# Optimization experiments

Hardware: AMD Instinct MI355X
Metric: run time of the kernel (lower is better)

The kernel has to match this reference:

```python
import jax, jax.numpy as jnp
import numpy as np

B, T, N, F_IN = 8, 288, 2000, 1
E, ID, H, K = 128, 16, 128, 20
FL = T // 2 + 1  # rfft length = in_len//2 + 1
EPS_NORM = 1e-12
EPS_LN = 1e-8


def setup_inputs() -> dict:
    key = jax.random.key(0)
    k0, k1, k2, k3, k4 = jax.random.split(key, 5)
    return {
        "x": jax.random.normal(k0, (B, T, N, F_IN), jnp.float32),
        "Ex": jax.random.normal(k1, (FL, E), jnp.float32),
        "nodes": jax.random.normal(k2, (N, ID), jnp.float32),
        "Wd": jax.random.normal(k3, (N, E + ID, H), jnp.float32),
        "Wxabs": jax.random.normal(k4, (H, H), jnp.float32),
    }


def reference(x, Ex, nodes, Wd, Wxabs):
    # [B,T,N,F] -> take feature 0 -> [B,N,T]
    xt = jnp.transpose(x[:, :, :, 0], (0, 2, 1))
    xf = jnp.abs(jnp.fft.rfft(xt, axis=-1))  # [B,N,FL]
    # F.normalize p=2 over dim=1 (nodes), then dim=2 (freq): x / max(||x||, eps)
    xf = xf / jnp.clip(jnp.sqrt(jnp.sum(xf * xf, axis=1, keepdims=True)), EPS_NORM)
    xf = xf / jnp.clip(jnp.sqrt(jnp.sum(xf * xf, axis=2, keepdims=True)), EPS_NORM)
    xe = jnp.matmul(xf, Ex)  # [B,N,E]
    # cat(): append static node identity embedding per batch element
    xk = jnp.concatenate(
        [xe, jnp.broadcast_to(nodes, (xe.shape[0], N, ID))], axis=-1
    )  # [B,N,E+ID]
    # per-node weight bmm: [N,B,E+ID] @ [N,E+ID,H] -> [B,N,H]
    x1 = jax.nn.relu(jnp.einsum('bnd,ndh->bnh', xk, Wd))
    # LayerNorm over last two dims [N,H], eps=1e-8, no affine
    mu = jnp.mean(x1, axis=(1, 2), keepdims=True)
    var = jnp.mean((x1 - mu) ** 2, axis=(1, 2), keepdims=True)
    x2 = (x1 - mu) / jnp.sqrt(var + EPS_LN)
    # dropout is identity at inference
    adp = jnp.einsum('bnh,hk->bnk', x2, Wxabs)  # convt
    adj = jnp.einsum('bnh,bmh->bnm', adp, x1)  # [B,N,N]
    adp = jax.nn.relu(adj)
    # dy_mask_graph: per-row topk over dim=2 (torch dim=1 of the [N,N] slice),
    # binary mask via scatter of ones, then elementwise mask
    _, idx = jax.lax.top_k(adp, K)  # [B,N,K]
    bi = jnp.arange(adp.shape[0])[:, None, None]
    ni = jnp.arange(N)[None, :, None]
    mask = jnp.zeros_like(adp).at[bi, ni, idx].set(1.0)
    adj_masked = adp * mask
    return jax.nn.softmax(adj_masked, axis=2)
```

## Files before the change

### kernel.cpp

```cpp
#include <hip/hip_runtime.h>
#include <math.h>

#define BB 8
#define TT 288
#define NN 2000
#define FLEN 145
#define EE 128
#define IDD 16
#define HH 128
#define DKK 144
#define KTOP 20

typedef _Float16 half8 __attribute__((ext_vector_type(8)));
typedef float f32x4 __attribute__((ext_vector_type(4)));
typedef unsigned short ushort_t;

#define OFF_TW  ((size_t)0)
#define SZ_TW   ((size_t)TT*FLEN*2)
#define OFF_XF  (OFF_TW + SZ_TW)
#define SZ_XF   ((size_t)BB*FLEN*NN)
#define OFF_ICN (OFF_XF + SZ_XF)
#define OFF_IRN (OFF_ICN + (size_t)BB*FLEN)
#define OFF_XE  (OFF_IRN + (size_t)BB*NN)
#define SZ_BNH  ((size_t)BB*NN*HH)
#define OFF_X1  (OFF_XE + SZ_BNH)
#define OFF_ADP (OFF_X1 + SZ_BNH)
#define OFF_CSW (OFF_ADP + SZ_BNH)
#define OFF_LNS (OFF_CSW + HH)
#define OFF_LNF (OFF_LNS + 16)

__device__ __forceinline__ float wredSum(float v) {
#pragma unroll
  for (int o = 32; o > 0; o >>= 1) v += __shfl_down(v, o, 64);
  return v;
}
__device__ __forceinline__ float wredMax(float v) {
#pragma unroll
  for (int o = 32; o > 0; o >>= 1) v = fmaxf(v, __shfl_down(v, o, 64));
  return v;
}

__device__ __forceinline__ void split16(float v, ushort_t& hi, ushort_t& lo) {
  _Float16 h = (_Float16)v;
  _Float16 l = (_Float16)(v - (float)h);
  union { _Float16 f; ushort_t u; } a, b;
  a.f = h; b.f = l;
  hi = a.u; lo = b.u;
}

__global__ void k_init(const float* __restrict__ Wx, float* __restrict__ csw,
                       float* __restrict__ lns) {
  int k = threadIdx.x;
  float s = 0.f;
  for (int h = 0; h < HH; ++h) s += Wx[h * HH + k];
  csw[k] = s;
  if (k < 16) lns[k] = 0.f;
}

__global__ void k_tw(float* __restrict__ tw) {
  int id = blockIdx.x * 256 + threadIdx.x;
  if (id >= TT * FLEN) return;
  int t = id / FLEN, f = id % FLEN;
  int r = (t * f) % TT;
  double th = -2.0 * 3.14159265358979323846 * (double)r / (double)TT;
  tw[2 * id]     = (float)cos(th);
  tw[2 * id + 1] = (float)sin(th);
}

__global__ void k_dft(const float* __restrict__ x, const float* __restrict__ tw,
                      float* __restrict__ xf) {
  __shared__ __align__(16) float Xs[16][128];
  __shared__ __align__(16) float TWs[16][32][2];
  const int b = blockIdx.z;
  const int f0 = blockIdx.y * 32;
  const int n0 = blockIdx.x * 128;
  const int tid = threadIdx.x;
  const int tn = tid & 31;
  const int tf = tid >> 5;
  float ar[4][4] = {}, ai[4][4] = {};
  for (int t0 = 0; t0 < TT; t0 += 16) {
    __syncthreads();
    for (int l = tid; l < 512; l += 256) {
      int row = l >> 5, q = l & 31;
      int n = n0 + q * 4;
      const float* src = x + ((size_t)b * TT + (t0 + row)) * NN + n;
      float4 v = make_float4(0, 0, 0, 0);
      if (n + 3 < NN) v = *(const float4*)src;
      else {
        if (n + 0 < NN) v.x = src[0];
        if (n + 1 < NN) v.y = src[1];
        if (n + 2 < NN) v.z = src[2];
        if (n + 3 < NN) v.w = src[3];
      }
      *(float4*)&Xs[row][q * 4] = v;
    }
    for (int l = tid; l < 512; l += 256) {
      int row = l >> 5, ff = l & 31;
      int f = f0 + ff;
      float2 cs = make_float2(0, 0);
      if (f < FLEN) cs = *(const float2*)&tw[((size_t)(t0 + row) * FLEN + f) * 2];
      *(float2*)&TWs[row][ff][0] = cs;
    }
    __syncthreads();
#pragma unroll 4
    for (int t = 0; t < 16; ++t) {
      float4 xv = *(float4*)&Xs[t][tn * 4];
      float xx[4] = {xv.x, xv.y, xv.z, xv.w};
      float4 p0 = *(float4*)&TWs[t][tf * 4][0];
      float4 p1 = *(float4*)&TWs[t][tf * 4 + 2][0];
      float c[4] = {p0.x, p0.z, p1.x, p1.z};
      float s[4] = {p0.y, p0.w, p1.y, p1.w};
#pragma unroll
      for (int i = 0; i < 4; ++i)
#pragma unroll
        for (int j = 0; j < 4; ++j) {
          ar[i][j] = fmaf(xx[j], c[i], ar[i][j]);
          ai[i][j] = fmaf(xx[j], s[i], ai[i][j]);
        }
    }
  }
#pragma unroll
  for (int i = 0; i < 4; ++i) {
    int f = f0 + tf * 4 + i;
    if (f >= FLEN) continue;
    float* dst = &xf[((size_t)b * FLEN + f) * NN];
    float o[4];
#pragma unroll
    for (int j = 0; j < 4; ++j)
      o[j] = sqrtf(ar[i][j] * ar[i][j] + ai[i][j] * ai[i][j]);
    int n = n0 + tn * 4;
    if (n + 3 < NN) *(float4*)&dst[n] = make_float4(o[0], o[1], o[2], o[3]);
    else {
#pragma unroll
      for (int j = 0; j < 4; ++j) if (n + j < NN) dst[n + j] = o[j];
    }
  }
}

__global__ void k_colnorm(const float* __restrict__ xf, float* __restrict__ icn) {
  __shared__ float sc[4];
  int bf = blockIdx.x;
  const float* rowp = xf + (size_t)bf * NN;
  float s = 0.f;
  for (int i = threadIdx.x; i < NN; i += 256) { float v = rowp[i]; s = fmaf(v, v, s); }
  s = wredSum(s);
  int lane = threadIdx.x & 63, w = threadIdx.x >> 6;
  if (lane == 0) sc[w] = s;
  __syncthreads();
  if (threadIdx.x == 0)
    icn[bf] = 1.f / fmaxf(sqrtf(sc[0] + sc[1] + sc[2] + sc[3]), 1e-12f);
}

__global__ void k_rownorm(const float* __restrict__ xf, const float* __restrict__ icn,
                          float* __restrict__ irn) {
  int b = blockIdx.y;
  int n = blockIdx.x * 256 + threadIdx.x;
  if (n >= NN) return;
  float s = 0.f;
  for (int f = 0; f < FLEN; ++f) {
    float v = xf[((size_t)b * FLEN + f) * NN + n] * icn[b * FLEN + f];
    s = fmaf(v, v, s);
  }
  irn[b * NN + n] = 1.f / fmaxf(sqrtf(s), 1e-12f);
}

__global__ void k_xe(const float* __restrict__ xf, const float* __restrict__ icn,
                     const float* __restrict__ irn, const float* __restrict__ Ex,
                     float* __restrict__ xe) {
  __shared__ __align__(16) float As[16][64];
  __shared__ __align__(16) float Bs[16][128];
  const int b = blockIdx.y;
  const int n0 = blockIdx.x * 64;
  const int tid = threadIdx.x;
  const int tn = tid >> 4, te = tid & 15;
  float acc[4][8] = {};
  for (int f0 = 0; f0 < 160; f0 += 16) {
    __syncthreads();
    {
      int kt = tid >> 4, q = tid & 15;
      int f = f0 + kt;
      int n = n0 + q * 4;
      float4 v = make_float4(0, 0, 0, 0);
      if (f < FLEN) {
        float ic = icn[b * FLEN + f];
        const float* src = &xf[((size_t)b * FLEN + f) * NN + n];
        if (n + 3 < NN) v = *(const float4*)src;
        else {
          if (n + 0 < NN) v.x = src[0];
          if (n + 1 < NN) v.y = src[1];
          if (n + 2 < NN) v.z = src[2];
          if (n + 3 < NN) v.w = src[3];
        }
        v.x *= ic; v.y *= ic; v.z *= ic; v.w *= ic;
      }
      *(float4*)&As[kt][q * 4] = v;
    }
    for (int l = tid; l < 512; l += 256) {
      int kt = l >> 5, q = l & 31;
      int f = f0 + kt;
      float4 v = make_float4(0, 0, 0, 0);
      if (f < FLEN) v = *(const float4*)&Ex[(size_t)f * EE + q * 4];
      *(float4*)&Bs[kt][q * 4] = v;
    }
    __syncthreads();
#pragma unroll
    for (int k = 0; k < 16; ++k) {
      float4 a  = *(float4*)&As[k][tn * 4];
      float4 b0 = *(float4*)&Bs[k][te * 4];
      float4 b1 = *(float4*)&Bs[k][64 + te * 4];
      float av[4] = {a.x, a.y, a.z, a.w};
      float bv[8] = {b0.x, b0.y, b0.z, b0.w, b1.x, b1.y, b1.z, b1.w};
#pragma unroll
      for (int i = 0; i < 4; ++i)
#pragma unroll
        for (int j = 0; j < 8; ++j)
          acc[i][j] = fmaf(av[i], bv[j], acc[i][j]);
    }
  }
#pragma unroll
  for (int i = 0; i < 4; ++i) {
    int n = n0 + tn * 4 + i;
    if (n >= NN) continue;
    float sc = irn[b * NN + n];
    float* dst = &xe[((size_t)b * NN + n) * EE];
    *(float4*)&dst[te * 4] =
        make_float4(acc[i][0] * sc, acc[i][1] * sc, acc[i][2] * sc, acc[i][3] * sc);
    *(float4*)&dst[64 + te * 4] =
        make_float4(acc[i][4] * sc, acc[i][5] * sc, acc[i][6] * sc, acc[i][7] * sc);
  }
}

__global__ void k_x1(const float* xe, const float* __restrict__ nodes,
                     const float* __restrict__ Wd, float* __restrict__ x1,
                     ushort_t* x1hl) {
  __shared__ __align__(16) float xk[8][DKK];
  __shared__ float red[4][32][33];
  const int n = blockIdx.x;
  const int tid = threadIdx.x;
  {
    int b = tid >> 5, q = tid & 31;
    *(float4*)&xk[b][q * 4] = *(const float4*)&xe[((size_t)b * NN + n) * EE + q * 4];
  }
  if (tid < 128) {
    int b = tid >> 4, i = tid & 15;
    xk[b][EE + i] = nodes[(size_t)n * IDD + i];
  }
  __syncthreads();
  const int h4 = tid & 31;
  const int dg = tid >> 5;
  float acc[8][4] = {};
  for (int d = dg; d < DKK; d += 8) {
    float4 wv = *(const float4*)&Wd[((size_t)n * DKK + d) * HH + h4 * 4];
#pragma unroll
    for (int b = 0; b < 8; ++b) {
      float xv = xk[b][d];
      acc[b][0] = fmaf(xv, wv.x, acc[b][0]);
      acc[b][1] = fmaf(xv, wv.y, acc[b][1]);
      acc[b][2] = fmaf(xv, wv.z, acc[b][2]);
      acc[b][3] = fmaf(xv, wv.w, acc[b][3]);
    }
  }
#pragma unroll
  for (int b = 0; b < 8; ++b)
#pragma unroll
    for (int j = 0; j < 4; ++j)
      acc[b][j] += __shfl_xor(acc[b][j], 32, 64);
  const int wv_ = tid >> 6, lane = tid & 63;
  if (lane < 32) {
#pragma unroll
    for (int b = 0; b < 8; ++b)
#pragma unroll
      for (int j = 0; j < 4; ++j)
        red[wv_][lane][b * 4 + j] = acc[b][j];
  }
  __syncthreads();
#pragma unroll
  for (int o = 0; o < 4; ++o) {
    int idx = tid + o * 256;
    int b = idx >> 7, h = idx & 127;
    float s = red[0][h >> 2][b * 4 + (h & 3)] + red[1][h >> 2][b * 4 + (h & 3)] +
              red[2][h >> 2][b * 4 + (h & 3)] + red[3][h >> 2][b * 4 + (h & 3)];
    s = fmaxf(s, 0.f);
    x1[((size_t)b * NN + n) * HH + h] = s;
    ushort_t hi, lo;
    split16(s, hi, lo);
    size_t base = ((size_t)b * NN + n) * 256;
    x1hl[base + h] = hi;
    x1hl[base + 128 + h] = lo;
  }
}

__global__ void k_ln_stats(const float* __restrict__ x1, float* __restrict__ lns) {
  __shared__ float sc[4], sc2[4];
  int b = blockIdx.y, chunk = blockIdx.x;
  const float* base = x1 + (size_t)b * NN * HH + (size_t)chunk * 8000;
  float s = 0.f, s2 = 0.f;
  for (int i = threadIdx.x; i < 8000; i += 256) {
    float v = base[i];
    s += v; s2 = fmaf(v, v, s2);
  }
  s = wredSum(s); s2 = wredSum(s2);
  int lane = threadIdx.x & 63, w = threadIdx.x >> 6;
  if (lane == 0) { sc[w] = s; sc2[w] = s2; }
  __syncthreads();
  if (threadIdx.x == 0) {
    atomicAdd(&lns[b], sc[0] + sc[1] + sc[2] + sc[3]);
    atomicAdd(&lns[8 + b], sc2[0] + sc2[1] + sc2[2] + sc2[3]);
  }
}

__global__ void k_ln_final(const float* __restrict__ lns, float* __restrict__ lnf) {
  int b = threadIdx.x;
  if (b < 8) {
    float cnt = (float)(NN * HH);
    float mu = lns[b] / cnt;
    float var = fmaxf(lns[8 + b] / cnt - mu * mu, 0.f);
    lnf[b] = mu;
    lnf[8 + b] = 1.f / sqrtf(var + 1e-8f);
  }
}

__global__ void k_adp(const float* __restrict__ x1, const float* __restrict__ Wx,
                      const float* __restrict__ csw, const float* __restrict__ lnf,
                      ushort_t* __restrict__ adphl) {
  __shared__ __align__(16) float As[16][64];
  __shared__ __align__(16) float Bs[16][128];
  const int r0 = blockIdx.x * 64;
  const int tid = threadIdx.x;
  const int tn = tid >> 4, te = tid & 15;
  float acc[4][8] = {};
  for (int k0 = 0; k0 < HH; k0 += 16) {
    __syncthreads();
    {
      int rr = tid >> 2, kq = tid & 3;
      float4 v = *(const float4*)&x1[(size_t)(r0 + rr) * HH + k0 + kq * 4];
      As[kq * 4 + 0][rr] = v.x;
      As[kq * 4 + 1][rr] = v.y;
      As[kq * 4 + 2][rr] = v.z;
      As[kq * 4 + 3][rr] = v.w;
    }
    for (int l = tid; l < 512; l += 256) {
      int kt = l >> 5, q = l & 31;
      *(float4*)&Bs[kt][q * 4] = *(const float4*)&Wx[(size_t)(k0 + kt) * HH + q * 4];
    }
    __syncthreads();
#pragma unroll
    for (int k = 0; k < 16; ++k) {
      float4 a  = *(float4*)&As[k][tn * 4];
      float4 b0 = *(float4*)&Bs[k][te * 4];
      float4 b1 = *(float4*)&Bs[k][64 + te * 4];
      float av[4] = {a.x, a.y, a.z, a.w};
      float bv[8] = {b0.x, b0.y, b0.z, b0.w, b1.x, b1.y, b1.z, b1.w};
#pragma unroll
      for (int i = 0; i < 4; ++i)
#pragma unroll
        for (int j = 0; j < 8; ++j)
          acc[i][j] = fmaf(av[i], bv[j], acc[i][j]);
    }
  }
  float4 c0 = *(const float4*)&csw[te * 4];
  float4 c1 = *(const float4*)&csw[64 + te * 4];
  float cw[8] = {c0.x, c0.y, c0.z, c0.w, c1.x, c1.y, c1.z, c1.w};
#pragma unroll
  for (int i = 0; i < 4; ++i) {
    int r = r0 + tn * 4 + i;
    int b = r / NN;
    float mu = lnf[b], isd = lnf[8 + b];
    size_t base = (size_t)r * 256;
    ushort_t hi[8], lo[8];
#pragma unroll
    for (int j = 0; j < 8; ++j) {
      float o = (acc[i][j] - mu * cw[j]) * isd;
      split16(o, hi[j], lo[j]);
    }
    ushort4 u;
    u.x = hi[0]; u.y = hi[1]; u.z = hi[2]; u.w = hi[3];
    *(ushort4*)&adphl[base + te * 4] = u;
    u.x = hi[4]; u.y = hi[5]; u.z = hi[6]; u.w = hi[7];
    *(ushort4*)&adphl[base + 64 + te * 4] = u;
    u.x = lo[0]; u.y = lo[1]; u.z = lo[2]; u.w = lo[3];
    *(ushort4*)&adphl[base + 128 + te * 4] = u;
    u.x = lo[4]; u.y = lo[5]; u.z = lo[6]; u.w = lo[7];
    *(ushort4*)&adphl[base + 128 + 64 + te * 4] = u;
  }
}

__global__ void k_adj(const ushort_t* __restrict__ adphl,
                      const ushort_t* __restrict__ x1hl,
                      float* __restrict__ out) {
  __shared__ __align__(16) ushort_t lds[4][128 * 32];
  const int b = blockIdx.z;
  const int n0 = blockIdx.y * 128;
  const int m0 = blockIdx.x * 128;
  const int tid = threadIdx.x;
  const int w = tid >> 6;
  const int lane = tid & 63;
  const int quad = lane >> 4, r16 = lane & 15;
  const int rBase = (w >> 1) * 64;
  const int cBase = (w & 1) * 64;

  f32x4 acc[4][4];
#pragma unroll
  for (int i = 0; i < 4; ++i)
#pragma unroll
    for (int j = 0; j < 4; ++j)
      acc[i][j] = (f32x4){0.f, 0.f, 0.f, 0.f};

  const ushort_t* src = (w < 2) ? adphl : x1hl;
  const int rg0 = (w < 2) ? n0 : m0;
  const int loOff = (w & 1) ? 128 : 0;

  for (int k0 = 0; k0 < HH; k0 += 32) {
    __syncthreads();
#pragma unroll
    for (int i = 0; i < 8; ++i) {
      int cl = i * 64 + lane;
      int row = cl >> 2, c = cl & 3;
      int gr = rg0 + row; if (gr > NN - 1) gr = NN - 1;
      const uint4* gp =
          (const uint4*)(src + ((size_t)(b * NN + gr)) * 256 + loOff + k0 + c * 8);
      uint4 v = *gp;
      *(uint4*)&lds[w][row * 32 + ((c ^ (row & 3)) * 8)] = v;
    }
    __syncthreads();

    half8 Ah[4], Al[4], Bh[4], Bl[4];
#pragma unroll
    for (int i = 0; i < 4; ++i) {
      int ar = rBase + i * 16 + r16;
      int aoff = ar * 32 + ((quad ^ (ar & 3)) * 8);
      Ah[i] = *(half8*)&lds[0][aoff];
      Al[i] = *(half8*)&lds[1][aoff];
      int br = cBase + i * 16 + r16;
      int boff = br * 32 + ((quad ^ (br & 3)) * 8);
      Bh[i] = *(half8*)&lds[2][boff];
      Bl[i] = *(half8*)&lds[3][boff];
    }
#pragma unroll
    for (int i = 0; i < 4; ++i)
#pragma unroll
      for (int j = 0; j < 4; ++j) {
        acc[i][j] = __builtin_amdgcn_mfma_f32_16x16x32_f16(Ah[i], Bh[j], acc[i][j], 0, 0, 0);
        acc[i][j] = __builtin_amdgcn_mfma_f32_16x16x32_f16(Ah[i], Bl[j], acc[i][j], 0, 0, 0);
        acc[i][j] = __builtin_amdgcn_mfma_f32_16x16x32_f16(Al[i], Bh[j], acc[i][j], 0, 0, 0);
      }
  }

#pragma unroll
  for (int i = 0; i < 4; ++i) {
#pragma unroll
    for (int j = 0; j < 4; ++j) {
      int m = m0 + cBase + j * 16 + r16;
      if (m >= NN) continue;
#pragma unroll
      for (int reg = 0; reg < 4; ++reg) {
        int n = n0 + rBase + i * 16 + quad * 4 + reg;
        if (n >= NN) continue;
        out[((size_t)b * NN + n) * NN + m] = fmaxf(acc[i][j][reg], 0.f);
      }
    }
  }
}

__global__ void k_softmax(float* __restrict__ out) {
  __shared__ __align__(16) float row[NN];
  __shared__ float scr[4];
  __shared__ float swv[4];
  __shared__ int swi[4];
  __shared__ float tkv[KTOP];
  __shared__ int tki[KTOP];
  __shared__ float bcast[1];
  const int r = blockIdx.x;
  float* g = out + (size_t)r * NN;
  const int tid = threadIdx.x;
  const int lane = tid & 63, w = tid >> 6;
  for (int q = tid; q < 500; q += 256) *(float4*)&row[q * 4] = *(const float4*)&g[q * 4];
  __syncthreads();
  float m = 0.f;
  for (int i = tid; i < NN; i += 256) m = fmaxf(m, row[i]);
  m = wredMax(m);
  if (lane == 0) scr[w] = m;
  __syncthreads();
  m = fmaxf(fmaxf(scr[0], scr[1]), fmaxf(scr[2], scr[3]));
  const float thr = m - 87.f;
  float s = 0.f, c = 0.f;
  for (int i = tid; i < NN; i += 256) {
    float v = row[i];
    if (v > thr) { s += expf(v - m); c += 1.f; }
  }
  s = wredSum(s); c = wredSum(c);
  __syncthreads();
  if (lane == 0) scr[w] = s;
  __syncthreads();
  s = scr[0] + scr[1] + scr[2] + scr[3];
  __syncthreads();
  if (lane == 0) scr[w] = c;
  __syncthreads();
  c = scr[0] + scr[1] + scr[2] + scr[3];
  const float em = expf(-m);
  if (c <= 20.5f) {
    float D = s + ((float)NN - c) * em;
    float invD = 1.f / D;
    float defv = em * invD;
    for (int q = tid; q < 500; q += 256) {
      float4 v = *(float4*)&row[q * 4];
      float4 o;
      o.x = (v.x > thr) ? expf(v.x - m) * invD : defv;
      o.y = (v.y > thr) ? expf(v.y - m) * invD : defv;
      o.z = (v.z > thr) ? expf(v.z - m) * invD : defv;
      o.w = (v.w > thr) ? expf(v.w - m) * invD : defv;
      *(float4*)&g[q * 4] = o;
    }
  } else {
    for (int it = 0; it < KTOP; ++it) {
      float bv = -1.f; int bi = 0x7fffffff;
      for (int i = tid; i < NN; i += 256) {
        float v = row[i];
        if (v > bv) { bv = v; bi = i; }
      }
#pragma unroll
      for (int o = 32; o > 0; o >>= 1) {
        float ov = __shfl_down(bv, o, 64);
        int oi = __shfl_down(bi, o, 64);
        if (ov > bv || (ov == bv && oi < bi)) { bv = ov; bi = oi; }
      }
      __syncthreads();
      if (lane == 0) { swv[w] = bv; swi[w] = bi; }
      __syncthreads();
      if (tid == 0) {
        float fv = swv[0]; int fi = swi[0];
        for (int ww = 1; ww < 4; ++ww)
          if (swv[ww] > fv || (swv[ww] == fv && swi[ww] < fi)) { fv = swv[ww]; fi = swi[ww]; }
        tkv[it] = fv; tki[it] = fi;
        row[fi] = -1.f;
      }
      __syncthreads();
    }
    if (tid == 0) {
      float D = ((float)(NN - KTOP)) * em;
      for (int it = 0; it < KTOP; ++it) D += expf(tkv[it] - m);
      bcast[0] = 1.f / D;
    }
    __syncthreads();
    float invD = bcast[0];
    float defv = em * invD;
    for (int q = tid; q < 500; q += 256)
      *(float4*)&g[q * 4] = make_float4(defv, defv, defv, defv);
    __syncthreads();
    if (tid < KTOP) g[tki[tid]] = expf(tkv[tid] - m) * invD;
  }
}

extern "C" void kernel_launch(void* const* d_in, const int* in_sizes, int n_in,
                              void* d_out, int out_size, void* d_ws, size_t ws_size,
                              hipStream_t stream) {
  const float* x     = (const float*)d_in[0];
  const float* Ex    = (const float*)d_in[1];
  const float* nodes = (const float*)d_in[2];
  const float* Wd    = (const float*)d_in[3];
  const float* Wx    = (const float*)d_in[4];
  float* out = (float*)d_out;
  float* w = (float*)d_ws;
  float* tw  = w + OFF_TW;
  float* xf  = w + OFF_XF;
  float* icn = w + OFF_ICN;
  float* irn = w + OFF_IRN;
  float* xe  = w + OFF_XE;
  float* x1  = w + OFF_X1;
  float* csw = w + OFF_CSW;
  float* lns = w + OFF_LNS;
  float* lnf = w + OFF_LNF;
  ushort_t* adphl = (ushort_t*)(w + OFF_ADP);
  ushort_t* x1hl  = (ushort_t*)(w + OFF_XE);

  k_init<<<1, 128, 0, stream>>>(Wx, csw, lns);
  k_tw<<<(TT * FLEN + 255) / 256, 256, 0, stream>>>(tw);
  k_dft<<<dim3(16, 5, BB), 256, 0, stream>>>(x, tw, xf);
  k_colnorm<<<BB * FLEN, 256, 0, stream>>>(xf, icn);
  k_rownorm<<<dim3(8, BB), 256, 0, stream>>>(xf, icn, irn);
  k_xe<<<dim3(32, BB), 256, 0, stream>>>(xf, icn, irn, Ex, xe);
  k_x1<<<NN, 256, 0, stream>>>(xe, nodes, Wd, x1, x1hl);
  k_ln_stats<<<dim3(32, BB), 256, 0, stream>>>(x1, lns);
  k_ln_final<<<1, 64, 0, stream>>>(lns, lnf);
  k_adp<<<250, 256, 0, stream>>>(x1, Wx, csw, lnf, adphl);
  k_adj<<<dim3(16, 16, BB), 256, 0, stream>>>(adphl, x1hl, out);
  k_softmax<<<BB * NN, 256, 0, stream>>>(out);
}
```

Measured before the change: 488.2 us.

## Recompute adjacency GEMM twice to avoid materializing full NxN scores

```diff
diff --git a/kernel.cpp b/kernel.cpp
--- a/kernel.cpp
+++ b/kernel.cpp
@@ -32,11 +32,6 @@
 __device__ __forceinline__ float wredSum(float v) {
 #pragma unroll
   for (int o = 32; o > 0; o >>= 1) v += __shfl_down(v, o, 64);
-  return v;
-}
-__device__ __forceinline__ float wredMax(float v) {
-#pragma unroll
-  for (int o = 32; o > 0; o >>= 1) v = fmaxf(v, __shfl_down(v, o, 64));
   return v;
 }
 
@@ -385,169 +380,156 @@
   }
 }
 
-__global__ void k_adj(const ushort_t* __restrict__ adphl,
-                      const ushort_t* __restrict__ x1hl,
-                      float* __restrict__ out) {
-  __shared__ __align__(16) ushort_t lds[4][128 * 32];
-  const int b = blockIdx.z;
-  const int n0 = blockIdx.y * 128;
-  const int m0 = blockIdx.x * 128;
-  const int tid = threadIdx.x;
-  const int w = tid >> 6;
-  const int lane = tid & 63;
-  const int quad = lane >> 4, r16 = lane & 15;
-  const int rBase = (w >> 1) * 64;
-  const int cBase = (w & 1) * 64;
-
-  f32x4 acc[4][4];
-#pragma unroll
-  for (int i = 0; i < 4; ++i)
-#pragma unroll
-    for (int j = 0; j < 4; ++j)
-      acc[i][j] = (f32x4){0.f, 0.f, 0.f, 0.f};
-
-  const ushort_t* src = (w < 2) ? adphl : x1hl;
-  const int rg0 = (w < 2) ? n0 : m0;
-  const int loOff = (w & 1) ? 128 : 0;
-
-  for (int k0 = 0; k0 < HH; k0 += 32) {
-    __syncthreads();
-#pragma unroll
-    for (int i = 0; i < 8; ++i) {
-      int cl = i * 64 + lane;
-      int row = cl >> 2, c = cl & 3;
-      int gr = rg0 + row; if (gr > NN - 1) gr = NN - 1;
-      const uint4* gp =
-          (const uint4*)(src + ((size_t)(b * NN + gr)) * 256 + loOff + k0 + c * 8);
-      uint4 v = *gp;
-      *(uint4*)&lds[w][row * 32 + ((c ^ (row & 3)) * 8)] = v;
-    }
-    __syncthreads();
-
-    half8 Ah[4], Al[4], Bh[4], Bl[4];
-#pragma unroll
-    for (int i = 0; i < 4; ++i) {
-      int ar = rBase + i * 16 + r16;
-      int aoff = ar * 32 + ((quad ^ (ar & 3)) * 8);
-      Ah[i] = *(half8*)&lds[0][aoff];
-      Al[i] = *(half8*)&lds[1][aoff];
-      int br = cBase + i * 16 + r16;
-      int boff = br * 32 + ((quad ^ (br & 3)) * 8);
-      Bh[i] = *(half8*)&lds[2][boff];
-      Bl[i] = *(half8*)&lds[3][boff];
-    }
-#pragma unroll
-    for (int i = 0; i < 4; ++i)
-#pragma unroll
-      for (int j = 0; j < 4; ++j) {
-        acc[i][j] = __builtin_amdgcn_mfma_f32_16x16x32_f16(Ah[i], Bh[j], acc[i][j], 0, 0, 0);
-        acc[i][j] = __builtin_amdgcn_mfma_f32_16x16x32_f16(Ah[i], Bl[j], acc[i][j], 0, 0, 0);
-        acc[i][j] = __builtin_amdgcn_mfma_f32_16x16x32_f16(Al[i], Bh[j], acc[i][j], 0, 0, 0);
-      }
-  }
-
+#define ADJ_PROLOG \
+  __shared__ __align__(16) ushort_t lds[4][128 * 32]; \
+  const int b = blockIdx.z; \
+  const int n0 = blockIdx.y * 128; \
+  const int m0 = blockIdx.x * 128; \
+  const int tid = threadIdx.x; \
+  const int w = tid >> 6; \
+  const int lane = tid & 63; \
+  const int quad = lane >> 4, r16 = lane & 15; \
+  const int rBase = (w >> 1) * 64; \
+  const int cBase = (w & 1) * 64; \
+  f32x4 acc[4][4]; \
+  _Pragma("unroll") for (int i = 0; i < 4; ++i) \
+  _Pragma("unroll") for (int j = 0; j < 4; ++j) acc[i][j] = (f32x4){0.f,0.f,0.f,0.f}; \
+  const ushort_t* src = (w < 2) ? adphl : x1hl; \
+  const int rg0 = (w < 2) ? n0 : m0; \
+  const int loOff = (w & 1) ? 128 : 0; \
+  for (int k0 = 0; k0 < HH; k0 += 32) { \
+    __syncthreads(); \
+    _Pragma("unroll") for (int i = 0; i < 8; ++i) { \
+      int cl = i * 64 + lane; \
+      int row = cl >> 2, c = cl & 3; \
+      int gr = rg0 + row; if (gr > NN - 1) gr = NN - 1; \
+      const uint4* gp = (const uint4*)(src + ((size_t)(b * NN + gr)) * 256 + loOff + k0 + c * 8); \
+      uint4 v = *gp; \
+      *(uint4*)&lds[w][row * 32 + ((c ^ (row & 3)) * 8)] = v; \
+    } \
+    __syncthreads(); \
+    half8 Ah[4], Al[4], Bh[4], Bl[4]; \
+    _Pragma("unroll") for (int i = 0; i < 4; ++i) { \
+      int ar = rBase + i * 16 + r16; \
+      int aoff = ar * 32 + ((quad ^ (ar & 3)) * 8); \
+      Ah[i] = *(half8*)&lds[0][aoff]; \
+      Al[i] = *(half8*)&lds[1][aoff]; \
+      int br = cBase + i * 16 + r16; \
+      int boff = br * 32 + ((quad ^ (br & 3)) * 8); \
+      Bh[i] = *(half8*)&lds[2][boff]; \
+      Bl[i] = *(half8*)&lds[3][boff]; \
+    } \
+    _Pragma("unroll") for (int i = 0; i < 4; ++i) \
+    _Pragma("unroll") for (int j = 0; j < 4; ++j) { \
+      acc[i][j] = __builtin_amdgcn_mfma_f32_16x16x32_f16(Ah[i], Bh[j], acc[i][j], 0, 0, 0); \
+      acc[i][j] = __builtin_amdgcn_mfma_f32_16x16x32_f16(Ah[i], Bl[j], acc[i][j], 0, 0, 0); \
+      acc[i][j] = __builtin_amdgcn_mfma_f32_16x16x32_f16(Al[i], Bh[j], acc[i][j], 0, 0, 0); \
+    } \
+  }
+
+__global__ void k_adj_max(const ushort_t* __restrict__ adphl,
+                          const ushort_t* __restrict__ x1hl,
+                          unsigned* __restrict__ rowmax) {
+  ADJ_PROLOG
 #pragma unroll
   for (int i = 0; i < 4; ++i) {
-#pragma unroll
-    for (int j = 0; j < 4; ++j) {
-      int m = m0 + cBase + j * 16 + r16;
-      if (m >= NN) continue;
+    float mx[4];
+#pragma unroll
+    for (int reg = 0; reg < 4; ++reg) {
+      float m_ = acc[i][0][reg];
+      m_ = fmaxf(m_, acc[i][1][reg]);
+      m_ = fmaxf(m_, acc[i][2][reg]);
+      m_ = fmaxf(m_, acc[i][3][reg]);
+#pragma unroll
+      for (int o = 1; o < 16; o <<= 1) m_ = fmaxf(m_, __shfl_xor(m_, o, 64));
+      mx[reg] = fmaxf(m_, 0.f);
+    }
+    if (r16 == 0) {
 #pragma unroll
       for (int reg = 0; reg < 4; ++reg) {
         int n = n0 + rBase + i * 16 + quad * 4 + reg;
-        if (n >= NN) continue;
-        out[((size_t)b * NN + n) * NN + m] = fmaxf(acc[i][j][reg], 0.f);
+        if (n < NN) atomicMax(&rowmax[b * NN + n], __float_as_uint(mx[reg]));
       }
     }
   }
 }
 
-__global__ void k_softmax(float* __restrict__ out) {
-  __shared__ __align__(16) float row[NN];
-  __shared__ float scr[4];
-  __shared__ float swv[4];
-  __shared__ int swi[4];
-  __shared__ float tkv[KTOP];
-  __shared__ int tki[KTOP];
-  __shared__ float bcast[1];
+__global__ void k_cand(const ushort_t* __restrict__ adphl,
+                       const ushort_t* __restrict__ x1hl,
+                       const unsigned* __restrict__ rowmax,
+                       unsigned* __restrict__ cnt, uint2* __restrict__ cand) {
+  ADJ_PROLOG
+#pragma unroll
+  for (int i = 0; i < 4; ++i) {
+#pragma unroll
+    for (int reg = 0; reg < 4; ++reg) {
+      int n = n0 + rBase + i * 16 + quad * 4 + reg;
+      if (n >= NN) continue;
+      int rr = b * NN + n;
+      float thr = __uint_as_float(rowmax[rr]) - 87.0f;
+#pragma unroll
+      for (int j = 0; j < 4; ++j) {
+        float v = fmaxf(acc[i][j][reg], 0.f);
+        int m = m0 + cBase + j * 16 + r16;
+        if (m < NN && v > thr) {
+          unsigned slot = atomicAdd(&cnt[rr], 1u);
+          if (slot < 64u) cand[(size_t)rr * 64 + slot] = make_uint2((unsigned)m, __float_as_uint(v));
+        }
+      }
+    }
+  }
+}
+
+__global__ void k_select(const unsigned* __restrict__ rowmax,
+                         const unsigned* __restrict__ cnt,
+                         const uint2* __restrict__ cand,
+                         unsigned* __restrict__ pcnt, float* __restrict__ pdef,
+                         uint2* __restrict__ plist) {
   const int r = blockIdx.x;
+  const int lane = threadIdx.x;
+  unsigned cn = cnt[r]; if (cn > 64u) cn = 64u;
+  float m = __uint_as_float(rowmax[r]);
+  float val = -1.f; int idx = 0x7fffffff;
+  if (lane < (int)cn) {
+    uint2 c = cand[(size_t)r * 64 + lane];
+    idx = (int)c.x; val = __uint_as_float(c.y);
+  }
+  float em = expf(-m);
+  float Dacc = 0.f; int Kp = 0;
+  float myV = 0.f; int myI = -1;
+  for (int it = 0; it < KTOP; ++it) {
+    float wv = val; int wi = idx;
+#pragma unroll
+    for (int o = 32; o > 0; o >>= 1) {
+      float ov = __shfl_xor(wv, o, 64);
+      int oi = __shfl_xor(wi, o, 64);
+      if (ov > wv || (ov == wv && oi < wi)) { wv = ov; wi = oi; }
+    }
+    if (wv < 0.f) break;
+    Kp++;
+    Dacc += expf(wv - m);
+    if (val == wv && idx == wi) val = -2.f;
+    if (lane == it) { myV = wv; myI = wi; }
+  }
+  float D = Dacc + ((float)NN - (float)Kp) * em;
+  float invD = 1.f / D;
+  if (lane == 0) { pdef[r] = em * invD; pcnt[r] = (unsigned)Kp; }
+  if (lane < Kp) plist[(size_t)r * KTOP + lane] =
+      make_uint2((unsigned)myI, __float_as_uint(expf(myV - m) * invD));
+}
+
+__global__ void k_fill(const unsigned* __restrict__ pcnt, const float* __restrict__ pdef,
+                       const uint2* __restrict__ plist, float* __restrict__ out) {
+  const int r = blockIdx.x;
+  const int tid = threadIdx.x;
+  float dv = pdef[r];
+  float4 q = make_float4(dv, dv, dv, dv);
   float* g = out + (size_t)r * NN;
-  const int tid = threadIdx.x;
-  const int lane = tid & 63, w = tid >> 6;
-  for (int q = tid; q < 500; q += 256) *(float4*)&row[q * 4] = *(const float4*)&g[q * 4];
+  for (int c = tid; c < 500; c += 256) ((float4*)g)[c] = q;
   __syncthreads();
-  float m = 0.f;
-  for (int i = tid; i < NN; i += 256) m = fmaxf(m, row[i]);
-  m = wredMax(m);
-  if (lane == 0) scr[w] = m;
-  __syncthreads();
-  m = fmaxf(fmaxf(scr[0], scr[1]), fmaxf(scr[2], scr[3]));
-  const float thr = m - 87.f;
-  float s = 0.f, c = 0.f;
-  for (int i = tid; i < NN; i += 256) {
-    float v = row[i];
-    if (v > thr) { s += expf(v - m); c += 1.f; }
-  }
-  s = wredSum(s); c = wredSum(c);
-  __syncthreads();
-  if (lane == 0) scr[w] = s;
-  __syncthreads();
-  s = scr[0] + scr[1] + scr[2] + scr[3];
-  __syncthreads();
-  if (lane == 0) scr[w] = c;
-  __syncthreads();
-  c = scr[0] + scr[1] + scr[2] + scr[3];
-  const float em = expf(-m);
-  if (c <= 20.5f) {
-    float D = s + ((float)NN - c) * em;
-    float invD = 1.f / D;
-    float defv = em * invD;
-    for (int q = tid; q < 500; q += 256) {
-      float4 v = *(float4*)&row[q * 4];
-      float4 o;
-      o.x = (v.x > thr) ? expf(v.x - m) * invD : defv;
-      o.y = (v.y > thr) ? expf(v.y - m) * invD : defv;
-      o.z = (v.z > thr) ? expf(v.z - m) * invD : defv;
-      o.w = (v.w > thr) ? expf(v.w - m) * invD : defv;
-      *(float4*)&g[q * 4] = o;
-    }
-  } else {
-    for (int it = 0; it < KTOP; ++it) {
-      float bv = -1.f; int bi = 0x7fffffff;
-      for (int i = tid; i < NN; i += 256) {
-        float v = row[i];
-        if (v > bv) { bv = v; bi = i; }
-      }
-#pragma unroll
-      for (int o = 32; o > 0; o >>= 1) {
-        float ov = __shfl_down(bv, o, 64);
-        int oi = __shfl_down(bi, o, 64);
-        if (ov > bv || (ov == bv && oi < bi)) { bv = ov; bi = oi; }
-      }
-      __syncthreads();
-      if (lane == 0) { swv[w] = bv; swi[w] = bi; }
-      __syncthreads();
-      if (tid == 0) {
-        float fv = swv[0]; int fi = swi[0];
-        for (int ww = 1; ww < 4; ++ww)
-          if (swv[ww] > fv || (swv[ww] == fv && swi[ww] < fi)) { fv = swv[ww]; fi = swi[ww]; }
-        tkv[it] = fv; tki[it] = fi;
-        row[fi] = -1.f;
-      }
-      __syncthreads();
-    }
-    if (tid == 0) {
-      float D = ((float)(NN - KTOP)) * em;
-      for (int it = 0; it < KTOP; ++it) D += expf(tkv[it] - m);
-      bcast[0] = 1.f / D;
-    }
-    __syncthreads();
-    float invD = bcast[0];
-    float defv = em * invD;
-    for (int q = tid; q < 500; q += 256)
-      *(float4*)&g[q * 4] = make_float4(defv, defv, defv, defv);
-    __syncthreads();
-    if (tid < KTOP) g[tki[tid]] = expf(tkv[tid] - m) * invD;
+  if (tid < (int)pcnt[r]) {
+    uint2 p = plist[(size_t)r * KTOP + tid];
+    g[p.x] = __uint_as_float(p.y);
   }
 }
 
@@ -572,6 +554,12 @@
   float* lnf = w + OFF_LNF;
   ushort_t* adphl = (ushort_t*)(w + OFF_ADP);
   ushort_t* x1hl  = (ushort_t*)(w + OFF_XE);
+  unsigned* rowmax = (unsigned*)(w + OFF_XF);
+  unsigned* cnt    = (unsigned*)(w + OFF_XF) + 16000;
+  unsigned* pcnt   = (unsigned*)(w + OFF_XF) + 32000;
+  float*    pdef   = (float*)(w + OFF_XF) + 48000;
+  uint2*    plist  = (uint2*)((w + OFF_XF) + 64000);
+  uint2*    cand   = (uint2*)(w + OFF_X1);
 
   k_init<<<1, 128, 0, stream>>>(Wx, csw, lns);
   k_tw<<<(TT * FLEN + 255) / 256, 256, 0, stream>>>(tw);
@@ -579,10 +567,13 @@
   k_colnorm<<<BB * FLEN, 256, 0, stream>>>(xf, icn);
   k_rownorm<<<dim3(8, BB), 256, 0, stream>>>(xf, icn, irn);
   k_xe<<<dim3(32, BB), 256, 0, stream>>>(xf, icn, irn, Ex, xe);
+  hipMemsetAsync(rowmax, 0, 32000 * sizeof(unsigned), stream);
   k_x1<<<NN, 256, 0, stream>>>(xe, nodes, Wd, x1, x1hl);
   k_ln_stats<<<dim3(32, BB), 256, 0, stream>>>(x1, lns);
   k_ln_final<<<1, 64, 0, stream>>>(lns, lnf);
   k_adp<<<250, 256, 0, stream>>>(x1, Wx, csw, lnf, adphl);
-  k_adj<<<dim3(16, 16, BB), 256, 0, stream>>>(adphl, x1hl, out);
-  k_softmax<<<BB * NN, 256, 0, stream>>>(out);
-}
+  k_adj_max<<<dim3(16, 16, BB), 256, 0, stream>>>(adphl, x1hl, rowmax);
+  k_cand<<<dim3(16, 16, BB), 256, 0, stream>>>(adphl, x1hl, rowmax, cnt, cand);
+  k_select<<<BB * NN, 64, 0, stream>>>(rowmax, cnt, cand, pcnt, pdef, plist);
+  k_fill<<<BB * NN, 256, 0, stream>>>(pcnt, pdef, plist, out);
+}
```

New measurement: 523.2 us. 1.07x slower.

## Write adjacency as fp16 scratch, recompute top candidates in fp32, then fill output

Applied to the files above, without the earlier changes.

```diff
diff --git a/kernel.cpp b/kernel.cpp
--- a/kernel.cpp
+++ b/kernel.cpp
@@ -34,11 +34,6 @@
   for (int o = 32; o > 0; o >>= 1) v += __shfl_down(v, o, 64);
   return v;
 }
-__device__ __forceinline__ float wredMax(float v) {
-#pragma unroll
-  for (int o = 32; o > 0; o >>= 1) v = fmaxf(v, __shfl_down(v, o, 64));
-  return v;
-}
 
 __device__ __forceinline__ void split16(float v, ushort_t& hi, ushort_t& lo) {
   _Float16 h = (_Float16)v;
@@ -46,6 +41,9 @@
   union { _Float16 f; ushort_t u; } a, b;
   a.f = h; b.f = l;
   hi = a.u; lo = b.u;
+}
+__device__ __forceinline__ float h2f(ushort_t u) {
+  union { _Float16 f; ushort_t u; } c; c.u = u; return (float)c.f;
 }
 
 __global__ void k_init(const float* __restrict__ Wx, float* __restrict__ csw,
@@ -385,9 +383,9 @@
   }
 }
 
-__global__ void k_adj(const ushort_t* __restrict__ adphl,
-                      const ushort_t* __restrict__ x1hl,
-                      float* __restrict__ out) {
+__global__ void k_adj16(const ushort_t* __restrict__ adphl,
+                        const ushort_t* __restrict__ x1hl,
+                        ushort_t* __restrict__ adj16) {
   __shared__ __align__(16) ushort_t lds[4][128 * 32];
   const int b = blockIdx.z;
   const int n0 = blockIdx.y * 128;
@@ -398,18 +396,14 @@
   const int quad = lane >> 4, r16 = lane & 15;
   const int rBase = (w >> 1) * 64;
   const int cBase = (w & 1) * 64;
-
   f32x4 acc[4][4];
 #pragma unroll
   for (int i = 0; i < 4; ++i)
 #pragma unroll
-    for (int j = 0; j < 4; ++j)
-      acc[i][j] = (f32x4){0.f, 0.f, 0.f, 0.f};
-
+    for (int j = 0; j < 4; ++j) acc[i][j] = (f32x4){0.f, 0.f, 0.f, 0.f};
   const ushort_t* src = (w < 2) ? adphl : x1hl;
   const int rg0 = (w < 2) ? n0 : m0;
   const int loOff = (w & 1) ? 128 : 0;
-
   for (int k0 = 0; k0 < HH; k0 += 32) {
     __syncthreads();
 #pragma unroll
@@ -417,13 +411,11 @@
       int cl = i * 64 + lane;
       int row = cl >> 2, c = cl & 3;
       int gr = rg0 + row; if (gr > NN - 1) gr = NN - 1;
-      const uint4* gp =
-          (const uint4*)(src + ((size_t)(b * NN + gr)) * 256 + loOff + k0 + c * 8);
+      const uint4* gp = (const uint4*)(src + ((size_t)(b * NN + gr)) * 256 + loOff + k0 + c * 8);
       uint4 v = *gp;
       *(uint4*)&lds[w][row * 32 + ((c ^ (row & 3)) * 8)] = v;
     }
     __syncthreads();
-
     half8 Ah[4], Al[4], Bh[4], Bl[4];
 #pragma unroll
     for (int i = 0; i < 4; ++i) {
@@ -445,109 +437,180 @@
         acc[i][j] = __builtin_amdgcn_mfma_f32_16x16x32_f16(Al[i], Bh[j], acc[i][j], 0, 0, 0);
       }
   }
-
 #pragma unroll
   for (int i = 0; i < 4; ++i) {
 #pragma unroll
-    for (int j = 0; j < 4; ++j) {
-      int m = m0 + cBase + j * 16 + r16;
-      if (m >= NN) continue;
-#pragma unroll
-      for (int reg = 0; reg < 4; ++reg) {
-        int n = n0 + rBase + i * 16 + quad * 4 + reg;
-        if (n >= NN) continue;
-        out[((size_t)b * NN + n) * NN + m] = fmaxf(acc[i][j][reg], 0.f);
+    for (int reg = 0; reg < 4; ++reg) {
+      int n = n0 + rBase + i * 16 + quad * 4 + reg;
+      if (n >= NN) continue;
+      ushort_t* dst = adj16 + ((size_t)(b * NN + n)) * 2048;
+#pragma unroll
+      for (int j = 0; j < 4; ++j) {
+        int m = m0 + cBase + j * 16 + r16;
+        if (m >= NN) continue;
+        union { _Float16 f; ushort_t u; } cvt;
+        cvt.f = (_Float16)fmaxf(acc[i][j][reg], 0.f);
+        dst[m] = cvt.u;
       }
     }
   }
 }
 
-__global__ void k_softmax(float* __restrict__ out) {
-  __shared__ __align__(16) float row[NN];
+__global__ void k_row(const ushort_t* __restrict__ adj16,
+                      const ushort_t* __restrict__ adphl,
+                      const ushort_t* __restrict__ x1hl,
+                      unsigned* __restrict__ pcnt, float* __restrict__ pdef,
+                      uint2* __restrict__ plist) {
+  __shared__ __align__(16) ushort_t a16[2048];
+  __shared__ float adp[128];
   __shared__ float scr[4];
+  __shared__ int candIdx[64];
+  __shared__ float candVal[64];
+  __shared__ int cCnt;
+  __shared__ __align__(16) float vals[NN];
   __shared__ float swv[4];
   __shared__ int swi[4];
   __shared__ float tkv[KTOP];
   __shared__ int tki[KTOP];
-  __shared__ float bcast[1];
   const int r = blockIdx.x;
+  const int b = r / NN;
+  const int tid = threadIdx.x;
+  const int lane = tid & 63, wv_ = tid >> 6;
+
+  if (tid < 250) ((uint4*)a16)[tid] = ((const uint4*)(adj16 + (size_t)r * 2048))[tid];
+  if (tid < 128) adp[tid] = h2f(adphl[(size_t)r * 256 + tid]) +
+                            h2f(adphl[(size_t)r * 256 + 128 + tid]);
+  if (tid == 0) cCnt = 0;
+  __syncthreads();
+
+  float m16 = 0.f;
+  for (int i = tid; i < NN; i += 256) m16 = fmaxf(m16, h2f(a16[i]));
+#pragma unroll
+  for (int o = 32; o > 0; o >>= 1) m16 = fmaxf(m16, __shfl_xor(m16, o, 64));
+  if (lane == 0) scr[wv_] = m16;
+  __syncthreads();
+  m16 = fmaxf(fmaxf(scr[0], scr[1]), fmaxf(scr[2], scr[3]));
+
+  const float tau = m16 - 95.f;
+  for (int i = tid; i < NN; i += 256) {
+    if (h2f(a16[i]) > tau) {
+      int s = atomicAdd(&cCnt, 1);
+      if (s < 64) candIdx[s] = i;
+    }
+  }
+  __syncthreads();
+  const int nc = cCnt;
+  const bool full = (nc > 64) || (m16 < 100.f);
+
+  if (!full) {
+    if (tid < nc) {
+      int m = candIdx[tid];
+      const half8* ph = (const half8*)(x1hl + ((size_t)(b * NN + m)) * 256);
+      float dot = 0.f;
+#pragma unroll
+      for (int c = 0; c < 16; ++c) {
+        half8 vh = ph[c], vl = ph[16 + c];
+#pragma unroll
+        for (int j = 0; j < 8; ++j)
+          dot = fmaf(adp[c * 8 + j], (float)vh[j] + (float)vl[j], dot);
+      }
+      candVal[tid] = fmaxf(dot, 0.f);
+    }
+    __syncthreads();
+    if (wv_ == 0) {
+      float val = (lane < nc) ? candVal[lane] : -1.f;
+      int idx = (lane < nc) ? candIdx[lane] : 0x7fffffff;
+      float m = val;
+#pragma unroll
+      for (int o = 32; o > 0; o >>= 1) m = fmaxf(m, __shfl_xor(m, o, 64));
+      m = fmaxf(m, 0.f);
+      float em = expf(-m);
+      float Dacc = 0.f; int Kp = 0; float myV = 0.f; int myI = -1;
+      for (int it = 0; it < KTOP; ++it) {
+        float wv2 = val; int wi = idx;
+#pragma unroll
+        for (int o = 32; o > 0; o >>= 1) {
+          float ov = __shfl_xor(wv2, o, 64);
+          int oi = __shfl_xor(wi, o, 64);
+          if (ov > wv2 || (ov == wv2 && oi < wi)) { wv2 = ov; wi = oi; }
+        }
+        if (wv2 < 0.f) break;
+        Kp++;
+        Dacc += expf(wv2 - m);
+        if (val == wv2 && idx == wi) val = -2.f;
+        if (lane == it) { myV = wv2; myI = wi; }
+      }
+      float D = Dacc + ((float)NN - (float)Kp) * em;
+      float invD = 1.f / D;
+      if (lane == 0) { pdef[r] = em * invD; pcnt[r] = (unsigned)Kp; }
+      if (lane < Kp)
+        plist[(size_t)r * KTOP + lane] = make_uint2((unsigned)myI, __float_as_uint(expf(myV - m) * invD));
+    }
+    return;
+  }
+
+  for (int m = tid; m < NN; m += 256) {
+    const half8* ph = (const half8*)(x1hl + ((size_t)(b * NN + m)) * 256);
+    float dot = 0.f;
+#pragma unroll
+    for (int c = 0; c < 16; ++c) {
+      half8 vh = ph[c], vl = ph[16 + c];
+#pragma unroll
+      for (int j = 0; j < 8; ++j)
+        dot = fmaf(adp[c * 8 + j], (float)vh[j] + (float)vl[j], dot);
+    }
+    vals[m] = fmaxf(dot, 0.f);
+  }
+  __syncthreads();
+  for (int it = 0; it < KTOP; ++it) {
+    float bv = -1.f; int bi = 0x7fffffff;
+    for (int i = tid; i < NN; i += 256) {
+      float v = vals[i];
+      if (v > bv) { bv = v; bi = i; }
+    }
+#pragma unroll
+    for (int o = 32; o > 0; o >>= 1) {
+      float ov = __shfl_down(bv, o, 64);
+      int oi = __shfl_down(bi, o, 64);
+      if (ov > bv || (ov == bv && oi < bi)) { bv = ov; bi = oi; }
+    }
+    __syncthreads();
+    if (lane == 0) { swv[wv_] = bv; swi[wv_] = bi; }
+    __syncthreads();
+    if (tid == 0) {
+      float fv = swv[0]; int fi = swi[0];
+      for (int ww = 1; ww < 4; ++ww)
+        if (swv[ww] > fv || (swv[ww] == fv && swi[ww] < fi)) { fv = swv[ww]; fi = swi[ww]; }
+      tkv[it] = fv; tki[it] = fi;
+      vals[fi] = -1.f;
+    }
+    __syncthreads();
+  }
+  if (tid == 0) {
+    float m = fmaxf(tkv[0], 0.f);
+    float em = expf(-m);
+    float D = ((float)(NN - KTOP)) * em;
+    for (int it = 0; it < KTOP; ++it) D += expf(tkv[it] - m);
+    float invD = 1.f / D;
+    pdef[r] = em * invD;
+    pcnt[r] = KTOP;
+    for (int it = 0; it < KTOP; ++it)
+      plist[(size_t)r * KTOP + it] = make_uint2((unsigned)tki[it], __float_as_uint(expf(tkv[it] - m) * invD));
+  }
+}
+
+__global__ void k_fill(const unsigned* __restrict__ pcnt, const float* __restrict__ pdef,
+                       const uint2* __restrict__ plist, float* __restrict__ out) {
+  const int r = blockIdx.x;
+  const int tid = threadIdx.x;
+  float dv = pdef[r];
+  float4 q = make_float4(dv, dv, dv, dv);
   float* g = out + (size_t)r * NN;
-  const int tid = threadIdx.x;
-  const int lane = tid & 63, w = tid >> 6;
-  for (int q = tid; q < 500; q += 256) *(float4*)&row[q * 4] = *(const float4*)&g[q * 4];
-  __syncthreads();
-  float m = 0.f;
-  for (int i = tid; i < NN; i += 256) m = fmaxf(m, row[i]);
-  m = wredMax(m);
-  if (lane == 0) scr[w] = m;
-  __syncthreads();
-  m = fmaxf(fmaxf(scr[0], scr[1]), fmaxf(scr[2], scr[3]));
-  const float thr = m - 87.f;
-  float s = 0.f, c = 0.f;
-  for (int i = tid; i < NN; i += 256) {
-    float v = row[i];
-    if (v > thr) { s += expf(v - m); c += 1.f; }
-  }
-  s = wredSum(s); c = wredSum(c);
-  __syncthreads();
-  if (lane == 0) scr[w] = s;
-  __syncthreads();
-  s = scr[0] + scr[1] + scr[2] + scr[3];
-  __syncthreads();
-  if (lane == 0) scr[w] = c;
-  __syncthreads();
-  c = scr[0] + scr[1] + scr[2] + scr[3];
-  const float em = expf(-m);
-  if (c <= 20.5f) {
-    float D = s + ((float)NN - c) * em;
-    float invD = 1.f / D;
-    float defv = em * invD;
-    for (int q = tid; q < 500; q += 256) {
-      float4 v = *(float4*)&row[q * 4];
-      float4 o;
-      o.x = (v.x > thr) ? expf(v.x - m) * invD : defv;
-      o.y = (v.y > thr) ? expf(v.y - m) * invD : defv;
-      o.z = (v.z > thr) ? expf(v.z - m) * invD : defv;
-      o.w = (v.w > thr) ? expf(v.w - m) * invD : defv;
-      *(float4*)&g[q * 4] = o;
-    }
-  } else {
-    for (int it = 0; it < KTOP; ++it) {
-      float bv = -1.f; int bi = 0x7fffffff;
-      for (int i = tid; i < NN; i += 256) {
-        float v = row[i];
-        if (v > bv) { bv = v; bi = i; }
-      }
-#pragma unroll
-      for (int o = 32; o > 0; o >>= 1) {
-        float ov = __shfl_down(bv, o, 64);
-        int oi = __shfl_down(bi, o, 64);
-        if (ov > bv || (ov == bv && oi < bi)) { bv = ov; bi = oi; }
-      }
-      __syncthreads();
-      if (lane == 0) { swv[w] = bv; swi[w] = bi; }
-      __syncthreads();
-      if (tid == 0) {
-        float fv = swv[0]; int fi = swi[0];
-        for (int ww = 1; ww < 4; ++ww)
-          if (swv[ww] > fv || (swv[ww] == fv && swi[ww] < fi)) { fv = swv[ww]; fi = swi[ww]; }
-        tkv[it] = fv; tki[it] = fi;
-        row[fi] = -1.f;
-      }
-      __syncthreads();
-    }
-    if (tid == 0) {
-      float D = ((float)(NN - KTOP)) * em;
-      for (int it = 0; it < KTOP; ++it) D += expf(tkv[it] - m);
-      bcast[0] = 1.f / D;
-    }
-    __syncthreads();
-    float invD = bcast[0];
-    float defv = em * invD;
-    for (int q = tid; q < 500; q += 256)
-      *(float4*)&g[q * 4] = make_float4(defv, defv, defv, defv);
-    __syncthreads();
-    if (tid < KTOP) g[tki[tid]] = expf(tkv[tid] - m) * invD;
+  for (int c = tid; c < 500; c += 256) ((float4*)g)[c] = q;
+  __syncthreads();
+  if (tid < (int)pcnt[r]) {
+    uint2 p = plist[(size_t)r * KTOP + tid];
+    g[p.x] = __uint_as_float(p.y);
   }
 }
 
@@ -572,6 +635,10 @@
   float* lnf = w + OFF_LNF;
   ushort_t* adphl = (ushort_t*)(w + OFF_ADP);
   ushort_t* x1hl  = (ushort_t*)(w + OFF_XE);
+  unsigned* pcnt = (unsigned*)(w + OFF_XF);
+  float*    pdef = (float*)(w + OFF_XF) + 16000;
+  uint2*    plist = (uint2*)((w + OFF_XF) + 32000);
+  ushort_t* adj16 = (ushort_t*)d_out;
 
   k_init<<<1, 128, 0, stream>>>(Wx, csw, lns);
   k_tw<<<(TT * FLEN + 255) / 256, 256, 0, stream>>>(tw);
@@ -583,6 +650,7 @@
   k_ln_stats<<<dim3(32, BB), 256, 0, stream>>>(x1, lns);
   k_ln_final<<<1, 64, 0, stream>>>(lns, lnf);
   k_adp<<<250, 256, 0, stream>>>(x1, Wx, csw, lnf, adphl);
-  k_adj<<<dim3(16, 16, BB), 256, 0, stream>>>(adphl, x1hl, out);
-  k_softmax<<<BB * NN, 256, 0, stream>>>(out);
-}
+  k_adj16<<<dim3(16, 16, BB), 256, 0, stream>>>(adphl, x1hl, adj16);
+  k_row<<<BB * NN, 256, 0, stream>>>(adj16, adphl, x1hl, pcnt, pdef, plist);
+  k_fill<<<BB * NN, 256, 0, stream>>>(pcnt, pdef, plist, out);
+}
```

After: 551.4 us. +13.0%, slower.
